# Optimization experiments

Hardware: AMD Instinct MI355X
Metric: run time of the kernel (lower is better)

The kernel has to match this reference:

```python
import jax, jax.numpy as jnp
import numpy as np
import math

N_HEAD = 12

def setup_inputs() -> dict:
    key = jax.random.key(0)
    ks = jax.random.split(key, 4)
    B, T, C = 4, 2048, 768
    x = jax.random.normal(ks[0], (B, T, C), dtype=jnp.float32)
    W_attn = jax.random.normal(ks[1], (C, 3 * C), dtype=jnp.float32) * (1.0 / math.sqrt(C))
    b_attn = jnp.zeros((3 * C,), dtype=jnp.float32)
    W_proj = jax.random.normal(ks[2], (C, C), dtype=jnp.float32) * (1.0 / math.sqrt(C))
    b_proj = jnp.zeros((C,), dtype=jnp.float32)
    decay_rates = jnp.full((N_HEAD,), 0.05, dtype=jnp.float32)
    return {"x": x, "W_attn": W_attn, "b_attn": b_attn,
            "W_proj": W_proj, "b_proj": b_proj, "decay_rates": decay_rates}

def reference(x, W_attn, b_attn, W_proj, b_proj, decay_rates):
    B, T, C = x.shape
    H = N_HEAD
    D = C // H
    qkv = x @ W_attn + b_attn                      # [B,T,3C]
    q, k, v = jnp.split(qkv, 3, axis=-1)
    q = q.reshape(B, T, H, D).transpose(0, 2, 1, 3)  # [B,H,T,D]
    k = k.reshape(B, T, H, D).transpose(0, 2, 1, 3)
    v = v.reshape(B, T, H, D).transpose(0, 2, 1, 3)
    att = jnp.einsum('bhqd,bhkd->bhqk', q, k) * (1.0 / math.sqrt(D))
    i = jnp.arange(T)[:, None]
    j = jnp.arange(T)[None, :]
    causal = i >= j                                  # [T,T]
    att = jnp.where(causal[None, None], att, -jnp.inf)
    att = jax.nn.softmax(att, axis=-1)
    # distances buffer: tril(j - i).abs() == (i - j) on the lower triangle, 0 above
    dist = jnp.where(causal, (i - j).astype(jnp.float32), 0.0)  # [T,T]
    decay = jnp.exp(-decay_rates[None, :, None, None] * dist[None, None])  # [1,H,T,T]
    att = att * decay
    att = att / (jnp.sum(att, axis=-1, keepdims=True) + 1e-8)
    y = jnp.einsum('bhqk,bhkd->bhqd', att, v)        # [B,H,T,D]
    y = y.transpose(0, 2, 1, 3).reshape(B, T, C)
    return y @ W_proj + b_proj
```

## Files before the change

### kernel.cpp

```cpp
#include <hip/hip_runtime.h>
#include <hip/hip_bf16.h>
#include <math.h>

#define T_ 2048
#define C_ 768
#define H_ 12
#define D_ 64
#define M_ 8192
#define QKV_N 2304

typedef short bf16x8 __attribute__((ext_vector_type(8)));
typedef float f32x4 __attribute__((ext_vector_type(4)));
typedef unsigned short u16;
typedef u16 u16x8 __attribute__((ext_vector_type(8)));
typedef u16 u16x4 __attribute__((ext_vector_type(4)));

__device__ u16 g_xb [M_*C_];
__device__ u16 g_wat[QKV_N*C_];
__device__ u16 g_wpt[C_*C_];
__device__ u16 g_q [M_*C_];
__device__ u16 g_k [M_*C_];
__device__ u16 g_vt[M_*C_];
__device__ u16 g_y [M_*C_];

__device__ __forceinline__ u16 f2bf(float f) {
    return __bfloat16_as_ushort(__float2bfloat16(f));
}
__device__ __forceinline__ f32x4 mfma16(bf16x8 a, bf16x8 b, f32x4 c) {
    return __builtin_amdgcn_mfma_f32_16x16x32_bf16(a, b, c, 0, 0, 0);
}
__device__ __forceinline__ void gl16(const u16* g, u16* l) {
    __builtin_amdgcn_global_load_lds(
        (const __attribute__((address_space(1))) unsigned int*)g,
        (__attribute__((address_space(3))) unsigned int*)l, 16, 0, 0);
}
__device__ __forceinline__ int ridx(int row, int chunk) {
    return row*64 + (((chunk) ^ (row & 7)) << 3);
}
__device__ __forceinline__ int swz(int row, int col) {
    return row*64 + ((((col >> 3) ^ (row & 7))) << 3) + (col & 7);
}

__global__ __launch_bounds__(256) void k_prep_x(const float* __restrict__ x)
{
    const int idx = blockIdx.x*256 + threadIdx.x;
    float4 a = ((const float4*)x)[idx*2];
    float4 b = ((const float4*)x)[idx*2+1];
    u16x8 o;
    o[0]=f2bf(a.x); o[1]=f2bf(a.y); o[2]=f2bf(a.z); o[3]=f2bf(a.w);
    o[4]=f2bf(b.x); o[5]=f2bf(b.y); o[6]=f2bf(b.z); o[7]=f2bf(b.w);
    ((u16x8*)g_xb)[idx] = o;
}

__global__ __launch_bounds__(256) void k_prep_wt(const float* __restrict__ src,
                                                 int which, int K, int N)
{
    __shared__ u16 L[64][72];
    const int tid = threadIdx.x;
    const int n0 = blockIdx.x*64, k0 = blockIdx.y*64;
    u16* dst = which ? g_wpt : g_wat;

    const int r  = tid >> 2;
    const int c0 = (tid & 3) * 16;
    const float* p = &src[(size_t)(k0 + r)*N + n0 + c0];
    float4 v[4];
    #pragma unroll
    for (int c = 0; c < 4; ++c) v[c] = ((const float4*)p)[c];
    const float* vf = (const float*)v;
    #pragma unroll
    for (int j = 0; j < 16; ++j) L[c0 + j][r] = f2bf(vf[j]);
    __syncthreads();
    const int nn = tid >> 2;
    const int s  = (tid & 3) * 16;
    *(u16x8*)&dst[(size_t)(n0+nn)*K + k0 + s]     = *(const u16x8*)&L[nn][s];
    *(u16x8*)&dst[(size_t)(n0+nn)*K + k0 + s + 8] = *(const u16x8*)&L[nn][s+8];
}

__global__ __launch_bounds__(256) void k_qkv(const float* __restrict__ bias)
{
    __shared__ u16 As[128*64];
    __shared__ u16 Bs[128*64];

    const int tid  = threadIdx.x;
    const int lane = tid & 63;
    const int wid  = tid >> 6;
    const int l15  = lane & 15;
    const int lg   = lane >> 4;
    const int wm = wid >> 1, wn = wid & 1;
    const int m0 = blockIdx.x * 128;
    const int n0 = blockIdx.y * 128;

    const int srow8 = lane >> 3;
    const int schk  = (lane & 7) ^ srow8;

    f32x4 acc[4][4];
    #pragma unroll
    for (int i = 0; i < 4; ++i)
        #pragma unroll
        for (int j = 0; j < 4; ++j) acc[i][j] = (f32x4){0.f,0.f,0.f,0.f};

    for (int k0 = 0; k0 < C_; k0 += 64) {
        __syncthreads();
        #pragma unroll
        for (int i = 0; i < 4; ++i) {
            const int r = wid*32 + i*8;
            gl16(&g_xb [(size_t)(m0 + r + srow8)*C_ + k0 + (schk<<3)], &As[r*64]);
            gl16(&g_wat[(size_t)(n0 + r + srow8)*C_ + k0 + (schk<<3)], &Bs[r*64]);
        }
        __syncthreads();
        #pragma unroll
        for (int kf = 0; kf < 2; ++kf) {
            bf16x8 bfr[4];
            #pragma unroll
            for (int nt = 0; nt < 4; ++nt) {
                const int rw = wn*64 + nt*16 + l15;
                bfr[nt] = *(const bf16x8*)&Bs[ridx(rw, kf*4 + lg)];
            }
            #pragma unroll
            for (int mt = 0; mt < 4; ++mt) {
                const int rw = wm*64 + mt*16 + l15;
                bf16x8 afr = *(const bf16x8*)&As[ridx(rw, kf*4 + lg)];
                #pragma unroll
                for (int nt = 0; nt < 4; ++nt)
                    acc[mt][nt] = mfma16(afr, bfr[nt], acc[mt][nt]);
            }
        }
    }

    const int nb    = n0 + wn*64;
    const int which = nb / C_;
    const int h     = (nb % C_) / D_;
    const int mbase = m0 + wm*64;
    const int bb    = mbase >> 11;
    const int bh    = bb*H_ + h;
    float bv4[4];
    #pragma unroll
    for (int nt = 0; nt < 4; ++nt) bv4[nt] = bias[nb + nt*16 + l15];

    if (which == 2) {
        #pragma unroll
        for (int mt = 0; mt < 4; ++mt) {
            const int tb = (mbase + mt*16 + lg*4) & (T_-1);
            #pragma unroll
            for (int nt = 0; nt < 4; ++nt) {
                const int d = nt*16 + l15;
                u16x4 pk;
                #pragma unroll
                for (int r = 0; r < 4; ++r) pk[r] = f2bf(acc[mt][nt][r] + bv4[nt]);
                *(u16x4*)&g_vt[((size_t)bh*D_ + d)*T_ + tb] = pk;
            }
        }
    } else {
        u16* dst = which ? g_k : g_q;
        #pragma unroll
        for (int mt = 0; mt < 4; ++mt)
            #pragma unroll
            for (int r = 0; r < 4; ++r) {
                const int t = (mbase + mt*16 + lg*4 + r) & (T_-1);
                #pragma unroll
                for (int nt = 0; nt < 4; ++nt)
                    dst[((size_t)bh*T_ + t)*D_ + nt*16 + l15] = f2bf(acc[mt][nt][r] + bv4[nt]);
            }
    }
}

__global__ __launch_bounds__(256) void k_attn(const float* __restrict__ rates)
{
    __shared__ u16 Ks[64*64];
    __shared__ u16 Vt[64*64];
    __shared__ u16 Ps[4][16*64];

    const int tid  = threadIdx.x;
    const int lane = tid & 63;
    const int wid  = tid >> 6;
    const int l15  = lane & 15;
    const int lg   = lane >> 4;

    const int id  = blockIdx.x;
    const int bh  = (id & 7)*6 + ((id >> 3) % 6);
    const int qt  = 31 - ((id >> 3) / 6);
    const int h   = bh % H_;
    const int bb  = bh / H_;
    const float rate = rates[h];
    const float LOG2E  = 1.4426950408889634f;
    const float srate  = rate * LOG2E;
    const float sscale = 0.125f * LOG2E;

    const int i0  = qt * 64;
    const int thr = wid*16 + l15;
    const int ig  = i0 + thr;

    const int wt = (int)(34.4f / (fmaxf(rate, 1e-8f) * 64.0f)) + 2;
    const int nT = min(qt + 1, wt);

    const u16* qb  = &g_q [(size_t)bh*T_*D_];
    const u16* kb  = &g_k [(size_t)bh*T_*D_];
    const u16* vtb = &g_vt[(size_t)bh*D_*T_];

    bf16x8 qf[2];
    qf[0] = *(const bf16x8*)&qb[(size_t)ig*D_ + lg*8];
    qf[1] = *(const bf16x8*)&qb[(size_t)ig*D_ + 32 + lg*8];

    float joff[16];
    #pragma unroll
    for (int t = 0; t < 4; ++t)
        #pragma unroll
        for (int r = 0; r < 4; ++r) joff[t*4+r] = srate * (float)(t*16 + lg*4 + r);

    f32x4 oAcc[4];
    #pragma unroll
    for (int n = 0; n < 4; ++n) oAcc[n] = (f32x4){0.f,0.f,0.f,0.f};
    float den = 0.f, mrow = 0.f;

    const int srow8 = lane >> 3;
    const int schk  = (lane & 7) ^ srow8;

    u16* PsW = &Ps[wid][0];

    for (int tt = 0; tt < nT; ++tt) {
        const int j0 = i0 - tt*64;
        __syncthreads();
        #pragma unroll
        for (int i = 0; i < 2; ++i) {
            const int r = wid*16 + i*8;
            gl16(&kb [(size_t)(j0 + r + srow8)*D_ + (schk<<3)], &Ks[r*64]);
            gl16(&vtb[(size_t)(r + srow8)*T_ + j0 + (schk<<3)], &Vt[r*64]);
        }
        __syncthreads();

        __builtin_amdgcn_s_setprio(1);
        f32x4 sAcc[4];
        #pragma unroll
        for (int t = 0; t < 4; ++t) sAcc[t] = (f32x4){0.f,0.f,0.f,0.f};
        #pragma unroll
        for (int t = 0; t < 4; ++t)
            #pragma unroll
            for (int kf = 0; kf < 2; ++kf) {
                bf16x8 kfr = *(const bf16x8*)&Ks[ridx(t*16 + l15, kf*4 + lg)];
                sAcc[t] = mfma16(kfr, qf[kf], sAcc[t]);
            }
        __builtin_amdgcn_s_setprio(0);

        float e[16];
        if (tt == 0) {
            const float sth = srate * (float)thr;
            float pv[16];
            float mx = -3e38f;
            #pragma unroll
            for (int t = 0; t < 4; ++t)
                #pragma unroll
                for (int r = 0; r < 4; ++r) {
                    const int jj = t*16 + lg*4 + r;
                    float v = fmaf(sAcc[t][r], sscale, joff[t*4+r] - sth);
                    if (jj > thr) v = -3e38f;
                    pv[t*4+r] = v;
                    mx = fmaxf(mx, v);
                }
            mx = fmaxf(mx, __shfl_xor(mx, 16, 64));
            mx = fmaxf(mx, __shfl_xor(mx, 32, 64));
            mrow = mx;
            #pragma unroll
            for (int i = 0; i < 16; ++i) {
                e[i] = __builtin_amdgcn_exp2f(pv[i] - mx);
                den += e[i];
            }
        } else {
            const float c0m = fmaf(srate, (float)(j0 - ig), -mrow);
            #pragma unroll
            for (int t = 0; t < 4; ++t)
                #pragma unroll
                for (int r = 0; r < 4; ++r) {
                    const float v = fmaf(sAcc[t][r], sscale, c0m + joff[t*4+r]);
                    const float p = __builtin_amdgcn_exp2f(v);
                    e[t*4+r] = p;
                    den += p;
                }
        }

        #pragma unroll
        for (int t = 0; t < 4; ++t) {
            u16x4 pk = { f2bf(e[t*4]), f2bf(e[t*4+1]), f2bf(e[t*4+2]), f2bf(e[t*4+3]) };
            *(u16x4*)&PsW[swz(l15, t*16 + lg*4)] = pk;
        }

        __builtin_amdgcn_s_setprio(1);
        #pragma unroll
        for (int kf = 0; kf < 2; ++kf) {
            bf16x8 pa = *(const bf16x8*)&PsW[ridx(l15, kf*4 + lg)];
            #pragma unroll
            for (int n = 0; n < 4; ++n) {
                bf16x8 vf = *(const bf16x8*)&Vt[ridx(n*16 + l15, kf*4 + lg)];
                oAcc[n] = mfma16(pa, vf, oAcc[n]);
            }
        }
        __builtin_amdgcn_s_setprio(0);
    }

    den += __shfl_xor(den, 16, 64);
    den += __shfl_xor(den, 32, 64);
    const float inv = 1.f / den;
    float ivr[4];
    #pragma unroll
    for (int r = 0; r < 4; ++r) ivr[r] = __shfl(inv, lg*4 + r, 64);
    #pragma unroll
    for (int r = 0; r < 4; ++r) {
        const int row = i0 + wid*16 + lg*4 + r;
        #pragma unroll
        for (int n = 0; n < 4; ++n)
            g_y[(size_t)(bb*T_ + row)*C_ + h*D_ + n*16 + l15] = f2bf(oAcc[n][r] * ivr[r]);
    }
}

__global__ __launch_bounds__(256) void k_proj(const float* __restrict__ bias,
                                              float* __restrict__ out)
{
    __shared__ u16 As[128*64];
    __shared__ u16 Bs[128*64];

    const int tid  = threadIdx.x;
    const int lane = tid & 63;
    const int wid  = tid >> 6;
    const int l15  = lane & 15;
    const int lg   = lane >> 4;
    const int wm = wid >> 1, wn = wid & 1;
    const int m0 = blockIdx.x * 128;
    const int n0 = blockIdx.y * 128;

    const int srow8 = lane >> 3;
    const int schk  = (lane & 7) ^ srow8;

    f32x4 acc[4][4];
    #pragma unroll
    for (int i = 0; i < 4; ++i)
        #pragma unroll
        for (int j = 0; j < 4; ++j) acc[i][j] = (f32x4){0.f,0.f,0.f,0.f};

    for (int k0 = 0; k0 < C_; k0 += 64) {
        __syncthreads();
        #pragma unroll
        for (int i = 0; i < 4; ++i) {
            const int r = wid*32 + i*8;
            gl16(&g_y  [(size_t)(m0 + r + srow8)*C_ + k0 + (schk<<3)], &As[r*64]);
            gl16(&g_wpt[(size_t)(n0 + r + srow8)*C_ + k0 + (schk<<3)], &Bs[r*64]);
        }
        __syncthreads();
        #pragma unroll
        for (int kf = 0; kf < 2; ++kf) {
            bf16x8 bfr[4];
            #pragma unroll
            for (int nt = 0; nt < 4; ++nt) {
                const int rw = wn*64 + nt*16 + l15;
                bfr[nt] = *(const bf16x8*)&Bs[ridx(rw, kf*4 + lg)];
            }
            #pragma unroll
            for (int mt = 0; mt < 4; ++mt) {
                const int rw = wm*64 + mt*16 + l15;
                bf16x8 afr = *(const bf16x8*)&As[ridx(rw, kf*4 + lg)];
                #pragma unroll
                for (int nt = 0; nt < 4; ++nt)
                    acc[mt][nt] = mfma16(afr, bfr[nt], acc[mt][nt]);
            }
        }
    }

    float bv4[4];
    #pragma unroll
    for (int nt = 0; nt < 4; ++nt) bv4[nt] = bias[n0 + wn*64 + nt*16 + l15];
    #pragma unroll
    for (int mt = 0; mt < 4; ++mt)
        #pragma unroll
        for (int r = 0; r < 4; ++r) {
            const int m = m0 + wm*64 + mt*16 + lg*4 + r;
            #pragma unroll
            for (int nt = 0; nt < 4; ++nt)
                out[(size_t)m*C_ + n0 + wn*64 + nt*16 + l15] = acc[mt][nt][r] + bv4[nt];
        }
}

extern "C" void kernel_launch(void* const* d_in, const int* in_sizes, int n_in,
                              void* d_out, int out_size, void* d_ws, size_t ws_size,
                              hipStream_t stream) {
    (void)in_sizes; (void)n_in; (void)d_ws; (void)ws_size; (void)out_size;
    const float* x      = (const float*)d_in[0];
    const float* W_attn = (const float*)d_in[1];
    const float* b_attn = (const float*)d_in[2];
    const float* W_proj = (const float*)d_in[3];
    const float* b_proj = (const float*)d_in[4];
    const float* rates  = (const float*)d_in[5];

    hipLaunchKernelGGL(k_prep_x,  dim3(M_*C_/8/256), dim3(256), 0, stream, x);
    hipLaunchKernelGGL(k_prep_wt, dim3(QKV_N/64, C_/64), dim3(256), 0, stream, W_attn, 0, C_, QKV_N);
    hipLaunchKernelGGL(k_prep_wt, dim3(C_/64,    C_/64), dim3(256), 0, stream, W_proj, 1, C_, C_);
    hipLaunchKernelGGL(k_qkv,  dim3(M_/128, QKV_N/128), dim3(256), 0, stream, b_attn);
    hipLaunchKernelGGL(k_attn, dim3(1536),              dim3(256), 0, stream, rates);
    hipLaunchKernelGGL(k_proj, dim3(M_/128, C_/128),    dim3(256), 0, stream, b_proj, (float*)d_out);
}
```

Baseline: 206.2 us.

## Double-buffer LDS tiles in GEMM and attention kernels; merge weight prep launches

Adds two-stage LDS double buffering to the QKV GEMM, the attention kernel and the projection GEMM. The next tile's global-to-LDS loads are issued before computing on the current tile, and one barrier per iteration replaces two. This is meant to hide global memory latency behind the MFMA work. The two weight-transpose launches are also merged into one grid to save a launch. Doubling the LDS footprint (64KB for the GEMMs) may lower occupancy.

```diff
diff --git a/kernel.cpp b/kernel.cpp
--- a/kernel.cpp
+++ b/kernel.cpp
@@ -52,13 +52,18 @@
     ((u16x8*)g_xb)[idx] = o;
 }
 
-__global__ __launch_bounds__(256) void k_prep_wt(const float* __restrict__ src,
-                                                 int which, int K, int N)
+__global__ __launch_bounds__(256) void k_prep_w(const float* __restrict__ Wa,
+                                                const float* __restrict__ Wp)
 {
     __shared__ u16 L[64][72];
     const int tid = threadIdx.x;
-    const int n0 = blockIdx.x*64, k0 = blockIdx.y*64;
+    const int bx  = blockIdx.x;
+    const int which = (bx >= QKV_N/64);
+    const float* src = which ? Wp : Wa;
+    const int N = which ? C_ : QKV_N;
     u16* dst = which ? g_wpt : g_wat;
+    const int n0 = (which ? bx - QKV_N/64 : bx) * 64;
+    const int k0 = blockIdx.y * 64;
 
     const int r  = tid >> 2;
     const int c0 = (tid & 3) * 16;
@@ -72,14 +77,14 @@
     __syncthreads();
     const int nn = tid >> 2;
     const int s  = (tid & 3) * 16;
-    *(u16x8*)&dst[(size_t)(n0+nn)*K + k0 + s]     = *(const u16x8*)&L[nn][s];
-    *(u16x8*)&dst[(size_t)(n0+nn)*K + k0 + s + 8] = *(const u16x8*)&L[nn][s+8];
+    *(u16x8*)&dst[(size_t)(n0+nn)*C_ + k0 + s]     = *(const u16x8*)&L[nn][s];
+    *(u16x8*)&dst[(size_t)(n0+nn)*C_ + k0 + s + 8] = *(const u16x8*)&L[nn][s+8];
 }
 
 __global__ __launch_bounds__(256) void k_qkv(const float* __restrict__ bias)
 {
-    __shared__ u16 As[128*64];
-    __shared__ u16 Bs[128*64];
+    __shared__ u16 As[2][128*64];
+    __shared__ u16 Bs[2][128*64];
 
     const int tid  = threadIdx.x;
     const int lane = tid & 63;
@@ -99,32 +104,49 @@
         #pragma unroll
         for (int j = 0; j < 4; ++j) acc[i][j] = (f32x4){0.f,0.f,0.f,0.f};
 
-    for (int k0 = 0; k0 < C_; k0 += 64) {
-        __syncthreads();
-        #pragma unroll
-        for (int i = 0; i < 4; ++i) {
-            const int r = wid*32 + i*8;
-            gl16(&g_xb [(size_t)(m0 + r + srow8)*C_ + k0 + (schk<<3)], &As[r*64]);
-            gl16(&g_wat[(size_t)(n0 + r + srow8)*C_ + k0 + (schk<<3)], &Bs[r*64]);
-        }
-        __syncthreads();
+    const u16* xa = &g_xb [(size_t)(m0 + wid*32 + srow8)*C_ + (schk<<3)];
+    const u16* wb = &g_wat[(size_t)(n0 + wid*32 + srow8)*C_ + (schk<<3)];
+
+    #pragma unroll
+    for (int i = 0; i < 4; ++i) {
+        const int r = wid*32 + i*8;
+        gl16(xa + (size_t)i*8*C_,       &As[0][r*64]);
+        gl16(wb + (size_t)i*8*C_,       &Bs[0][r*64]);
+    }
+    __syncthreads();
+
+    int cur = 0;
+    for (int k = 0; k < 12; ++k) {
+        if (k < 11) {
+            const int ko = (k+1)*64;
+            #pragma unroll
+            for (int i = 0; i < 4; ++i) {
+                const int r = wid*32 + i*8;
+                gl16(xa + (size_t)i*8*C_ + ko, &As[cur^1][r*64]);
+                gl16(wb + (size_t)i*8*C_ + ko, &Bs[cur^1][r*64]);
+            }
+        }
+        __builtin_amdgcn_s_setprio(1);
         #pragma unroll
         for (int kf = 0; kf < 2; ++kf) {
             bf16x8 bfr[4];
             #pragma unroll
             for (int nt = 0; nt < 4; ++nt) {
                 const int rw = wn*64 + nt*16 + l15;
-                bfr[nt] = *(const bf16x8*)&Bs[ridx(rw, kf*4 + lg)];
+                bfr[nt] = *(const bf16x8*)&Bs[cur][ridx(rw, kf*4 + lg)];
             }
             #pragma unroll
             for (int mt = 0; mt < 4; ++mt) {
                 const int rw = wm*64 + mt*16 + l15;
-                bf16x8 afr = *(const bf16x8*)&As[ridx(rw, kf*4 + lg)];
+                bf16x8 afr = *(const bf16x8*)&As[cur][ridx(rw, kf*4 + lg)];
                 #pragma unroll
                 for (int nt = 0; nt < 4; ++nt)
                     acc[mt][nt] = mfma16(afr, bfr[nt], acc[mt][nt]);
             }
         }
+        __builtin_amdgcn_s_setprio(0);
+        __syncthreads();
+        cur ^= 1;
     }
 
     const int nb    = n0 + wn*64;
@@ -166,8 +188,8 @@
 
 __global__ __launch_bounds__(256) void k_attn(const float* __restrict__ rates)
 {
-    __shared__ u16 Ks[64*64];
-    __shared__ u16 Vt[64*64];
+    __shared__ u16 Ks[2][64*64];
+    __shared__ u16 Vt[2][64*64];
     __shared__ u16 Ps[4][16*64];
 
     const int tid  = threadIdx.x;
@@ -217,16 +239,26 @@
 
     u16* PsW = &Ps[wid][0];
 
+    #pragma unroll
+    for (int i = 0; i < 2; ++i) {
+        const int r = wid*16 + i*8;
+        gl16(&kb [(size_t)(i0 + r + srow8)*D_ + (schk<<3)], &Ks[0][r*64]);
+        gl16(&vtb[(size_t)(r + srow8)*T_ + i0 + (schk<<3)], &Vt[0][r*64]);
+    }
+    __syncthreads();
+
+    int cur = 0;
     for (int tt = 0; tt < nT; ++tt) {
         const int j0 = i0 - tt*64;
-        __syncthreads();
-        #pragma unroll
-        for (int i = 0; i < 2; ++i) {
-            const int r = wid*16 + i*8;
-            gl16(&kb [(size_t)(j0 + r + srow8)*D_ + (schk<<3)], &Ks[r*64]);
-            gl16(&vtb[(size_t)(r + srow8)*T_ + j0 + (schk<<3)], &Vt[r*64]);
-        }
-        __syncthreads();
+        if (tt + 1 < nT) {
+            const int jn = j0 - 64;
+            #pragma unroll
+            for (int i = 0; i < 2; ++i) {
+                const int r = wid*16 + i*8;
+                gl16(&kb [(size_t)(jn + r + srow8)*D_ + (schk<<3)], &Ks[cur^1][r*64]);
+                gl16(&vtb[(size_t)(r + srow8)*T_ + jn + (schk<<3)], &Vt[cur^1][r*64]);
+            }
+        }
 
         __builtin_amdgcn_s_setprio(1);
         f32x4 sAcc[4];
@@ -236,7 +268,7 @@
         for (int t = 0; t < 4; ++t)
             #pragma unroll
             for (int kf = 0; kf < 2; ++kf) {
-                bf16x8 kfr = *(const bf16x8*)&Ks[ridx(t*16 + l15, kf*4 + lg)];
+                bf16x8 kfr = *(const bf16x8*)&Ks[cur][ridx(t*16 + l15, kf*4 + lg)];
                 sAcc[t] = mfma16(kfr, qf[kf], sAcc[t]);
             }
         __builtin_amdgcn_s_setprio(0);
@@ -289,11 +321,13 @@
             bf16x8 pa = *(const bf16x8*)&PsW[ridx(l15, kf*4 + lg)];
             #pragma unroll
             for (int n = 0; n < 4; ++n) {
-                bf16x8 vf = *(const bf16x8*)&Vt[ridx(n*16 + l15, kf*4 + lg)];
+                bf16x8 vf = *(const bf16x8*)&Vt[cur][ridx(n*16 + l15, kf*4 + lg)];
                 oAcc[n] = mfma16(pa, vf, oAcc[n]);
             }
         }
         __builtin_amdgcn_s_setprio(0);
+        __syncthreads();
+        cur ^= 1;
     }
 
     den += __shfl_xor(den, 16, 64);
@@ -314,8 +348,8 @@
 __global__ __launch_bounds__(256) void k_proj(const float* __restrict__ bias,
                                               float* __restrict__ out)
 {
-    __shared__ u16 As[128*64];
-    __shared__ u16 Bs[128*64];
+    __shared__ u16 As[2][128*64];
+    __shared__ u16 Bs[2][128*64];
 
     const int tid  = threadIdx.x;
     const int lane = tid & 63;
@@ -335,32 +369,49 @@
         #pragma unroll
         for (int j = 0; j < 4; ++j) acc[i][j] = (f32x4){0.f,0.f,0.f,0.f};
 
-    for (int k0 = 0; k0 < C_; k0 += 64) {
-        __syncthreads();
-        #pragma unroll
-        for (int i = 0; i < 4; ++i) {
-            const int r = wid*32 + i*8;
-            gl16(&g_y  [(size_t)(m0 + r + srow8)*C_ + k0 + (schk<<3)], &As[r*64]);
-            gl16(&g_wpt[(size_t)(n0 + r + srow8)*C_ + k0 + (schk<<3)], &Bs[r*64]);
-        }
-        __syncthreads();
+    const u16* ya = &g_y  [(size_t)(m0 + wid*32 + srow8)*C_ + (schk<<3)];
+    const u16* wb = &g_wpt[(size_t)(n0 + wid*32 + srow8)*C_ + (schk<<3)];
+
+    #pragma unroll
+    for (int i = 0; i < 4; ++i) {
+        const int r = wid*32 + i*8;
+        gl16(ya + (size_t)i*8*C_, &As[0][r*64]);
+        gl16(wb + (size_t)i*8*C_, &Bs[0][r*64]);
+    }
+    __syncthreads();
+
+    int cur = 0;
+    for (int k = 0; k < 12; ++k) {
+        if (k < 11) {
+            const int ko = (k+1)*64;
+            #pragma unroll
+            for (int i = 0; i < 4; ++i) {
+                const int r = wid*32 + i*8;
+                gl16(ya + (size_t)i*8*C_ + ko, &As[cur^1][r*64]);
+                gl16(wb + (size_t)i*8*C_ + ko, &Bs[cur^1][r*64]);
+            }
+        }
+        __builtin_amdgcn_s_setprio(1);
         #pragma unroll
         for (int kf = 0; kf < 2; ++kf) {
             bf16x8 bfr[4];
             #pragma unroll
             for (int nt = 0; nt < 4; ++nt) {
                 const int rw = wn*64 + nt*16 + l15;
-                bfr[nt] = *(const bf16x8*)&Bs[ridx(rw, kf*4 + lg)];
+                bfr[nt] = *(const bf16x8*)&Bs[cur][ridx(rw, kf*4 + lg)];
             }
             #pragma unroll
             for (int mt = 0; mt < 4; ++mt) {
                 const int rw = wm*64 + mt*16 + l15;
-                bf16x8 afr = *(const bf16x8*)&As[ridx(rw, kf*4 + lg)];
+                bf16x8 afr = *(const bf16x8*)&As[cur][ridx(rw, kf*4 + lg)];
                 #pragma unroll
                 for (int nt = 0; nt < 4; ++nt)
                     acc[mt][nt] = mfma16(afr, bfr[nt], acc[mt][nt]);
             }
         }
+        __builtin_amdgcn_s_setprio(0);
+        __syncthreads();
+        cur ^= 1;
     }
 
     float bv4[4];
@@ -388,9 +439,8 @@
     const float* b_proj = (const float*)d_in[4];
     const float* rates  = (const float*)d_in[5];
 
-    hipLaunchKernelGGL(k_prep_x,  dim3(M_*C_/8/256), dim3(256), 0, stream, x);
-    hipLaunchKernelGGL(k_prep_wt, dim3(QKV_N/64, C_/64), dim3(256), 0, stream, W_attn, 0, C_, QKV_N);
-    hipLaunchKernelGGL(k_prep_wt, dim3(C_/64,    C_/64), dim3(256), 0, stream, W_proj, 1, C_, C_);
+    hipLaunchKernelGGL(k_prep_x, dim3(M_*C_/8/256), dim3(256), 0, stream, x);
+    hipLaunchKernelGGL(k_prep_w, dim3(QKV_N/64 + C_/64, C_/64), dim3(256), 0, stream, W_attn, W_proj);
     hipLaunchKernelGGL(k_qkv,  dim3(M_/128, QKV_N/128), dim3(256), 0, stream, b_attn);
     hipLaunchKernelGGL(k_attn, dim3(1536),              dim3(256), 0, stream, rates);
     hipLaunchKernelGGL(k_proj, dim3(M_/128, C_/128),    dim3(256), 0, stream, b_proj, (float*)d_out);
```

Result: faster. 196.1 us (-4.9%).
